# Kernel tuning notes

Hardware: AMD Instinct MI355X
Metric: run time of the kernel (lower is better)

Reference implementation:

```python
import jax, jax.numpy as jnp
import numpy as np

H = 4  # attention heads


def _lstm(x, Wih, Whh, b, reverse=False):
    # x: [N, L, din] -> hidden sequence [N, L, dh]; PyTorch gate order i,f,g,o
    if reverse:
        x = x[:, ::-1, :]
    xT = jnp.swapaxes(x, 0, 1)  # [L, N, din]
    dh = Whh.shape[1]
    N = x.shape[0]

    def step(carry, xt):
        h, c = carry
        z = xt @ Wih.T + h @ Whh.T + b
        i, f, g, o = jnp.split(z, 4, axis=-1)
        c = jax.nn.sigmoid(f) * c + jax.nn.sigmoid(i) * jnp.tanh(g)
        h = jax.nn.sigmoid(o) * jnp.tanh(c)
        return (h, c), h

    h0 = jnp.zeros((N, dh), x.dtype)
    _, hs = jax.lax.scan(step, (h0, h0), xT)
    hs = jnp.swapaxes(hs, 0, 1)
    if reverse:
        hs = hs[:, ::-1, :]
    return hs


def setup_inputs() -> dict:
    key = jax.random.key(0)
    ks = jax.random.split(key, 24)
    B, T, D = 8, 128, 512
    C, L, U, V, E = 1000, 8, 16, 5000, 256

    def w(k, shape, fan_in):
        return jax.random.normal(k, shape, jnp.float32) * (1.0 / np.sqrt(fan_in))

    inp = {
        'model_embed': jax.random.normal(ks[0], (B, T, D), jnp.float32),
        'emb_table': w(ks[1], (V, E), E),
        'ctx_Wih_f': w(ks[2], (4 * E, E), E),
        'ctx_Whh_f': w(ks[3], (4 * E, E), E),
        'ctx_b_f': jnp.zeros((4 * E,), jnp.float32),
        'ctx_Wih_b': w(ks[4], (4 * E, E), E),
        'ctx_Whh_b': w(ks[5], (4 * E, E), E),
        'ctx_b_b': jnp.zeros((4 * E,), jnp.float32),
        'ctx_out_W': w(ks[6], (D, 2 * E), 2 * E),
        'hist_Wih': w(ks[7], (4 * D, D), D),
        'hist_Whh': w(ks[8], (4 * D, D), D),
        'hist_b': jnp.zeros((4 * D,), jnp.float32),
        'hist_out_W': w(ks[9], (D, D), D),
        'Wq': w(ks[10], (D, D), D),
        'Wk': w(ks[11], (D, D), D),
        'Wv': w(ks[12], (D, D), D),
        'Wo': w(ks[13], (D, D), D),
        'acoustic_W': w(ks[14], (D, D), D),
        'context_idxs': jax.random.randint(ks[15], (C, L), 0, V),
        'context_history_idx': jax.random.randint(ks[16], (B, U), 0, C),
        'context_ilens': jax.random.randint(ks[17], (C,), 1, L + 1),
        'context_history_ilens': jax.random.randint(ks[18], (B,), 1, U + 1),
    }
    return inp


def reference(model_embed, emb_table, ctx_Wih_f, ctx_Whh_f, ctx_b_f,
              ctx_Wih_b, ctx_Whh_b, ctx_b_b, ctx_out_W,
              hist_Wih, hist_Whh, hist_b, hist_out_W,
              Wq, Wk, Wv, Wo, acoustic_W,
              context_idxs, context_history_idx, context_ilens,
              context_history_ilens):
    C, L = context_idxs.shape
    B, T, D = model_embed.shape
    U = context_history_idx.shape[1]

    # --- ContextEncoderBiLSTM: embed -> BiLSTM -> proj -> length-masked mean ---
    emb = emb_table[context_idxs]                               # [C, L, E]
    hf = _lstm(emb, ctx_Wih_f, ctx_Whh_f, ctx_b_f)
    hb = _lstm(emb, ctx_Wih_b, ctx_Whh_b, ctx_b_b, reverse=True)
    seq = jnp.concatenate([hf, hb], -1) @ ctx_out_W.T           # [C, L, D]
    m = (jnp.arange(L)[None, :] < context_ilens[:, None]).astype(seq.dtype)
    ctx_mean = (seq * m[..., None]).sum(1) / context_ilens[:, None].astype(seq.dtype)  # [C, D]

    # --- history gather + ContextHistoryEncoderLSTM ---
    hist_in = ctx_mean[context_history_idx.reshape(-1)].reshape(B, U, D)
    hist = _lstm(hist_in, hist_Wih, hist_Whh, hist_b) @ hist_out_W.T  # [B, U, D]

    # --- fuse acoustic + history, attention-based adapter ---
    mp = model_embed @ acoustic_W.T                             # [B, T, D]
    fused = (mp[:, :, None, :] + hist[:, None, :, :]).reshape(B, T * U, D)
    dh = D // H
    q = (fused @ Wq.T).reshape(B, T * U, H, dh)
    k = (ctx_mean @ Wk.T).reshape(C, H, dh)
    v = (ctx_mean @ Wv.T).reshape(C, H, dh)
    scores = jnp.einsum('bqhd,chd->bhqc', q, k) / jnp.sqrt(jnp.asarray(dh, q.dtype))
    attn = jax.nn.softmax(scores, axis=-1)                      # [B, H, TU, C]
    out = (jnp.einsum('bhqc,chd->bqhd', attn, v).reshape(B, T * U, D) @ Wo.T)
    out = out.reshape(B, T, U, D)
    prob = attn.reshape(B, H, T, U, C).mean(1)                  # [B, T, U, C]
    logit = scores.reshape(B, H, T, U, C).mean(1)

    # --- batch greedy monotonic decoding (scan over T, full length) ---
    probT = jnp.moveaxis(prob, 1, 0)                            # [T, B, U, C]
    outT = jnp.moveaxis(out, 1, 0)                              # [T, B, U, D]
    b_idx = jnp.arange(B)

    def step(u, inp):
        p_t, o_t = inp
        u_c = jnp.minimum(u, U - 1)
        valid_u = jnp.minimum(u + 1, U - 1)
        tok = context_history_idx[b_idx, valid_u]
        blank_p = p_t[b_idx, u_c, 0]
        tok_p = p_t[b_idx, u_c, tok]
        upd = (tok_p > blank_p).astype(jnp.int32)
        return u_c + upd, (u_c, o_t[b_idx, u_c])

    u0 = jnp.zeros((B,), jnp.int32)
    _, (idx, o) = jax.lax.scan(step, u0, (probT, outT))
    o = jnp.moveaxis(o, 0, 1)                                   # [B, T, D]
    return o, logit, prob
```

## Files before the change

kernel.cpp:

```cpp
#include <hip/hip_runtime.h>
#include <math.h>

namespace {
constexpr int B_ = 8, T_ = 128, D_ = 512, C_ = 1000, L_ = 8, U_ = 16, E_ = 256, H_ = 4;
constexpr int VOC_ = 5000;
constexpr int DH_ = D_ / H_;
constexpr int E4_ = 4 * E_;
constexpr int D4_ = 4 * D_;
constexpr int TU_ = T_ * U_;
constexpr int HC_ = H_ * C_;
constexpr float SCALE_ = 0.088388347648318447f;

constexpr int XZ_NB  = E4_ / 64;
constexpr int XZ_MB  = (VOC_ + 63) / 64;
constexpr int XZ_NWG = XZ_NB * XZ_MB;
constexpr int XZ_CPX = XZ_NWG / 8;

constexpr size_t XZ_    = 0;
constexpr size_t SM_    = 0;
constexpr size_t SH_    = SM_ + (size_t)B_ * T_ * HC_;
constexpr size_t AOUT_  = SH_ + (size_t)B_ * U_ * HC_;
constexpr size_t PVP_   = AOUT_ + (size_t)B_ * T_ * D_;
constexpr size_t REG_A  = 2ul * VOC_ * E4_;
constexpr size_t HPING  = REG_A;
constexpr size_t CST    = HPING + 2ul * C_ * E_;
constexpr size_t HPONG  = CST + 2ul * C_ * E_;
constexpr size_t HFALL  = HPONG + 2ul * C_ * E_;
constexpr size_t HBALL  = HFALL + (size_t)C_ * L_ * E_;
constexpr size_t CATM   = HBALL + (size_t)C_ * L_ * E_;
constexpr size_t CTXM   = CATM + (size_t)C_ * 2 * E_;
constexpr size_t KWS    = CTXM + (size_t)C_ * D_;
constexpr size_t VWS    = KWS + (size_t)C_ * D_;
constexpr size_t WQA    = VWS + (size_t)C_ * D_;
constexpr size_t WQH    = WQA + (size_t)D_ * D_;
constexpr size_t HXP    = WQH + (size_t)D_ * D_;
constexpr size_t HALL   = HXP + (size_t)B_ * U_ * D4_;
constexpr size_t HGLOB  = HALL + (size_t)B_ * U_ * D_;
constexpr size_t HG2    = HGLOB + (size_t)B_ * D_;
constexpr size_t HISTC  = HG2 + (size_t)B_ * D_;
constexpr size_t QM_    = HISTC + (size_t)B_ * D_;
constexpr size_t QH_    = QM_ + (size_t)B_ * T_ * D_;
constexpr size_t SMSUM  = QH_ + (size_t)B_ * U_ * D_;
constexpr size_t SHSUM  = SMSUM + (size_t)B_ * T_ * C_;
constexpr size_t DEN_   = SHSUM + (size_t)B_ * U_ * C_;
constexpr size_t BITS_  = DEN_ + (size_t)B_ * T_ * U_ * H_;
constexpr size_t USEL_  = BITS_ + 4096;
constexpr size_t PERM_  = USEL_ + (size_t)B_ * T_;
constexpr size_t NACT_  = PERM_ + C_;
constexpr size_t WS_NEED = NACT_ + 8;
}

__device__ __forceinline__ float fsig(float x)  { return 1.f / (1.f + __expf(-x)); }
__device__ __forceinline__ float ftanh(float x) { return 1.f - 2.f / (__expf(2.f * x) + 1.f); }
__device__ __forceinline__ void fma4(float4& a, float w, const float4& v) {
  a.x += w * v.x; a.y += w * v.y; a.z += w * v.z; a.w += w * v.w;
}

struct GemmP {
  const float* A1; int lda1;
  const int* ridx; int ridx_stride; int ridx_off;
  const float* W1; int ldw1;
  const float* bias;
  float* out; int ldc;
  int M, N, K;
  float scale;
  int a_zoff, w_zoff, c_zoff;
};

template <int TN>
__device__ __forceinline__ void gemm_core(const GemmP& g, int z, int by, int bx) {
  constexpr int UN = TN / 16;
  constexpr int WP = TN / 64;
  __shared__ float As[16][68];
  __shared__ float Ws[16][TN + 4];
  const int m0 = by * 64;
  const int n0 = bx * TN;
  if (m0 >= g.M || n0 >= g.N) return;
  const float* A1 = g.A1 + (long)z * g.a_zoff;
  const float* W1 = g.W1 + (long)z * g.w_zoff;
  float* out = g.out + (long)z * g.c_zoff;
  const int tid = threadIdx.x;
  const int tx = tid & 15, ty = tid >> 4;
  const int sr = tid >> 2, skq = (tid & 3) * 4;
  float acc[4][UN] = {};
  int sarow = -1;
  {
    const int gm = m0 + sr;
    if (gm < g.M) sarow = g.ridx ? g.ridx[gm * g.ridx_stride + g.ridx_off] : gm;
  }
  float4 pa, pw[WP];
  {
    pa = make_float4(0.f, 0.f, 0.f, 0.f);
    if (sarow >= 0) pa = *(const float4*)&A1[(long)sarow * g.lda1 + skq];
#pragma unroll
    for (int p = 0; p < WP; ++p) {
      const int gn = n0 + sr + p * 64;
      pw[p] = make_float4(0.f, 0.f, 0.f, 0.f);
      if (gn < g.N) pw[p] = *(const float4*)&W1[(long)gn * g.ldw1 + skq];
    }
  }
  for (int k0 = 0; k0 < g.K; k0 += 16) {
    As[skq][sr] = pa.x; As[skq + 1][sr] = pa.y; As[skq + 2][sr] = pa.z; As[skq + 3][sr] = pa.w;
#pragma unroll
    for (int p = 0; p < WP; ++p) {
      const int r = sr + p * 64;
      Ws[skq][r] = pw[p].x; Ws[skq + 1][r] = pw[p].y; Ws[skq + 2][r] = pw[p].z; Ws[skq + 3][r] = pw[p].w;
    }
    __syncthreads();
    const int kn = k0 + 16;
    if (kn < g.K) {
      pa = make_float4(0.f, 0.f, 0.f, 0.f);
      if (sarow >= 0) pa = *(const float4*)&A1[(long)sarow * g.lda1 + kn + skq];
#pragma unroll
      for (int p = 0; p < WP; ++p) {
        const int gn = n0 + sr + p * 64;
        pw[p] = make_float4(0.f, 0.f, 0.f, 0.f);
        if (gn < g.N) pw[p] = *(const float4*)&W1[(long)gn * g.ldw1 + kn + skq];
      }
    }
#pragma unroll
    for (int k = 0; k < 16; ++k) {
      const float4 a = *(const float4*)&As[k][ty * 4];
#pragma unroll
      for (int q = 0; q < UN / 4; ++q) {
        const float4 w = *(const float4*)&Ws[k][q * 64 + tx * 4];
        acc[0][q*4+0] += a.x * w.x; acc[0][q*4+1] += a.x * w.y; acc[0][q*4+2] += a.x * w.z; acc[0][q*4+3] += a.x * w.w;
        acc[1][q*4+0] += a.y * w.x; acc[1][q*4+1] += a.y * w.y; acc[1][q*4+2] += a.y * w.z; acc[1][q*4+3] += a.y * w.w;
        acc[2][q*4+0] += a.z * w.x; acc[2][q*4+1] += a.z * w.y; acc[2][q*4+2] += a.z * w.z; acc[2][q*4+3] += a.z * w.w;
        acc[3][q*4+0] += a.w * w.x; acc[3][q*4+1] += a.w * w.y; acc[3][q*4+2] += a.w * w.z; acc[3][q*4+3] += a.w * w.w;
      }
    }
    __syncthreads();
  }
#pragma unroll
  for (int i = 0; i < 4; ++i) {
    const int gm = m0 + ty * 4 + i;
    if (gm >= g.M) continue;
#pragma unroll
    for (int q = 0; q < UN / 4; ++q) {
#pragma unroll
      for (int j = 0; j < 4; ++j) {
        const int gn = n0 + q * 64 + tx * 4 + j;
        if (gn >= g.N) continue;
        float v2 = acc[i][q*4+j];
        if (g.bias) v2 += g.bias[gn];
        out[(long)gm * g.ldc + gn] = v2 * g.scale;
      }
    }
  }
}

__global__ __launch_bounds__(256) void k_gemm64(GemmP p)  { gemm_core<64>(p, blockIdx.z, blockIdx.y, blockIdx.x); }
__global__ __launch_bounds__(256) void k_gemm64x2(GemmP p0, GemmP p1, int zs) {
  int z = blockIdx.z;
  if (z < zs) gemm_core<64>(p0, z, blockIdx.y, blockIdx.x);
  else gemm_core<64>(p1, z - zs, blockIdx.y, blockIdx.x);
}
__global__ __launch_bounds__(256) void k_gemm64x3(GemmP p0, GemmP p1, GemmP p2) {
  int z = blockIdx.z;
  if (z == 0) gemm_core<64>(p0, 0, blockIdx.y, blockIdx.x);
  else if (z == 1) gemm_core<64>(p1, 0, blockIdx.y, blockIdx.x);
  else gemm_core<64>(p2, 0, blockIdx.y, blockIdx.x);
}
__global__ __launch_bounds__(256) void k_gemm128x2(GemmP p0, GemmP p1, int zs) {
  int z = blockIdx.z;
  if (z < zs) gemm_core<128>(p0, z, blockIdx.y, blockIdx.x);
  else gemm_core<128>(p1, z - zs, blockIdx.y, blockIdx.x);
}
__global__ __launch_bounds__(256) void k_gemm64xcd(GemmP p0, GemmP p1) {
  const int bid = blockIdx.x;
  const int logical = (bid & 7) * XZ_CPX + (bid >> 3);
  const int bx = logical % XZ_NB;
  const int by = logical / XZ_NB;
  if (blockIdx.z == 0) gemm_core<64>(p0, 0, by, bx);
  else gemm_core<64>(p1, 0, by, bx);
}

__global__ __launch_bounds__(256) void k_gemm_nn(
    const float* __restrict__ A0, const float* __restrict__ B0, float* __restrict__ O0,
    const float* __restrict__ A1, const float* __restrict__ B1, float* __restrict__ O1) {
  const float* A = blockIdx.z ? A1 : A0;
  const float* B = blockIdx.z ? B1 : B0;
  float* O = blockIdx.z ? O1 : O0;
  __shared__ float As[16][68];
  __shared__ float Bs[16][68];
  const int m0 = blockIdx.y * 64, n0 = blockIdx.x * 64;
  const int tid = threadIdx.x;
  const int tx = tid & 15, ty = tid >> 4;
  const int sr = tid >> 2, skq = (tid & 3) * 4;
  float acc[4][4] = {};
  for (int k0 = 0; k0 < 512; k0 += 16) {
    {
      float4 v = *(const float4*)&A[(long)(m0 + sr) * 512 + k0 + skq];
      As[skq][sr] = v.x; As[skq + 1][sr] = v.y; As[skq + 2][sr] = v.z; As[skq + 3][sr] = v.w;
    }
#pragma unroll
    for (int p = 0; p < 4; ++p) {
      int idx = tid + p * 256;
      int kk = idx >> 6, jj = idx & 63;
      Bs[kk][jj] = B[(long)(k0 + kk) * 512 + n0 + jj];
    }
    __syncthreads();
#pragma unroll
    for (int k = 0; k < 16; ++k) {
      const float4 a = *(const float4*)&As[k][ty * 4];
      const float4 w = *(const float4*)&Bs[k][tx * 4];
      acc[0][0] += a.x * w.x; acc[0][1] += a.x * w.y; acc[0][2] += a.x * w.z; acc[0][3] += a.x * w.w;
      acc[1][0] += a.y * w.x; acc[1][1] += a.y * w.y; acc[1][2] += a.y * w.z; acc[1][3] += a.y * w.w;
      acc[2][0] += a.z * w.x; acc[2][1] += a.z * w.y; acc[2][2] += a.z * w.z; acc[2][3] += a.z * w.w;
      acc[3][0] += a.w * w.x; acc[3][1] += a.w * w.y; acc[3][2] += a.w * w.z; acc[3][3] += a.w * w.w;
    }
    __syncthreads();
  }
#pragma unroll
  for (int i = 0; i < 4; ++i)
#pragma unroll
    for (int j = 0; j < 4; ++j)
      O[(long)(m0 + ty * 4 + i) * 512 + n0 + tx * 4 + j] = acc[i][j];
}

__global__ __launch_bounds__(256) void k_perm(
    const int* __restrict__ ilens, int* __restrict__ perm, int* __restrict__ nact) {
  __shared__ int cnt[9];
  __shared__ int start[9];
  const int tid = threadIdx.x;
  if (tid < 9) cnt[tid] = 0;
  __syncthreads();
  for (int c = tid; c < C_; c += 256) atomicAdd(&cnt[ilens[c]], 1);
  __syncthreads();
  if (tid == 0) {
    int acc = 0;
    for (int k = 8; k >= 0; --k) { start[k] = acc; if (k > 0) acc += cnt[k]; }
    for (int t = 0; t < 8; ++t) nact[t] = start[t];
  }
  __syncthreads();
  const int wave = tid >> 6, lane = tid & 63;
  for (int k = wave + 1; k <= 8; k += 4) {
    int base = start[k];
    for (int c0 = 0; c0 < C_; c0 += 64) {
      int c = c0 + lane;
      bool f = (c < C_) && (ilens[c] == k);
      unsigned long long m = __ballot(f);
      if (f) {
        int r = __popcll(m & ((1ull << lane) - 1ull));
        perm[base + r] = c;
      }
      base += __popcll(m);
    }
  }
}

__global__ __launch_bounds__(256) void k_ctx_step(
    const float* __restrict__ xz, const int* __restrict__ ctx_idxs,
    const float* __restrict__ Whh_f, const float* __restrict__ Whh_b,
    const float* __restrict__ h_prev, float* __restrict__ h_next,
    float* __restrict__ c_st,
    float* __restrict__ hf_all, float* __restrict__ hb_all,
    const int* __restrict__ perm, const int* __restrict__ nactArr, int t) {
  __shared__ float Hs[32][20];
  __shared__ float Wg[4][32][68];
  __shared__ float zb[4][16][68];
  const int e0 = blockIdx.x * 64;
  const int c0 = blockIdx.y * 16;
  const int dir = blockIdx.z;
  int nact = C_;
  if (dir == 0) {
    nact = nactArr[t];
    if (c0 >= nact) return;
  }
  const int tid = threadIdx.x;
  const float* Whh = dir ? Whh_b : Whh_f;
  const float* hp = h_prev + (size_t)dir * C_ * E_;
  const int gp = tid >> 7;
  const int rem = tid & 127;
  const int cy = rem >> 4;
  const int ex = rem & 15;
  const bool hstage = (tid < 128);
  const int hcr = tid & 15, hkq = ((tid >> 4) & 7) * 4;
  const int hc = c0 + hcr;
  int hrow = -1;
  if (dir == 0) { if (hc < nact) hrow = perm[hc]; }
  else if (hc < C_) hrow = hc;
  float4 acc4[2][2];
  acc4[0][0] = acc4[0][1] = acc4[1][0] = acc4[1][1] = make_float4(0.f, 0.f, 0.f, 0.f);
  float4 phv = make_float4(0.f, 0.f, 0.f, 0.f);
  float4 pwv[8];
  if (hstage && hrow >= 0) phv = *(const float4*)&hp[(size_t)hrow * E_ + hkq];
#pragma unroll
  for (int p = 0; p < 8; ++p) {
    int idx = tid + p * 256;
    int ee = idx & 63, kq = ((idx >> 6) & 7) * 4, gg = idx >> 9;
    pwv[p] = *(const float4*)&Whh[(size_t)(gg * E_ + e0 + ee) * E_ + kq];
  }
  for (int k0 = 0; k0 < E_; k0 += 32) {
    if (hstage) {
      Hs[hkq][hcr] = phv.x; Hs[hkq + 1][hcr] = phv.y; Hs[hkq + 2][hcr] = phv.z; Hs[hkq + 3][hcr] = phv.w;
    }
#pragma unroll
    for (int p = 0; p < 8; ++p) {
      int idx = tid + p * 256;
      int ee = idx & 63, kq = ((idx >> 6) & 7) * 4, gg = idx >> 9;
      Wg[gg][kq][ee] = pwv[p].x; Wg[gg][kq + 1][ee] = pwv[p].y; Wg[gg][kq + 2][ee] = pwv[p].z; Wg[gg][kq + 3][ee] = pwv[p].w;
    }
    __syncthreads();
    const int kn = k0 + 32;
    if (kn < E_) {
      phv = make_float4(0.f, 0.f, 0.f, 0.f);
      if (hstage && hrow >= 0) phv = *(const float4*)&hp[(size_t)hrow * E_ + kn + hkq];
#pragma unroll
      for (int p = 0; p < 8; ++p) {
        int idx = tid + p * 256;
        int ee = idx & 63, kq = ((idx >> 6) & 7) * 4, gg = idx >> 9;
        pwv[p] = *(const float4*)&Whh[(size_t)(gg * E_ + e0 + ee) * E_ + kn + kq];
      }
    }
#pragma unroll
    for (int kk = 0; kk < 32; ++kk) {
      const float a0 = Hs[kk][cy * 2];
      const float a1 = Hs[kk][cy * 2 + 1];
#pragma unroll
      for (int gg = 0; gg < 2; ++gg) {
        const float4 w = *(const float4*)&Wg[gp * 2 + gg][kk][ex * 4];
        fma4(acc4[gg][0], a0, w);
        fma4(acc4[gg][1], a1, w);
      }
    }
    __syncthreads();
  }
#pragma unroll
  for (int gg = 0; gg < 2; ++gg) {
    *(float4*)&zb[gp * 2 + gg][cy * 2 + 0][ex * 4] = acc4[gg][0];
    *(float4*)&zb[gp * 2 + gg][cy * 2 + 1][ex * 4] = acc4[gg][1];
  }
  __syncthreads();
  const int lpos = dir ? (L_ - 1 - t) : t;
  const float* xz_dir = xz + (size_t)dir * VOC_ * E4_;
  float* c_state = c_st + (size_t)dir * C_ * E_;
  float* hn_out = h_next + (size_t)dir * C_ * E_;
  float* hall = dir ? hb_all : hf_all;
  const int oc = tid >> 4, oe = (tid & 15) * 4;
  const int lc = c0 + oc;
  int c = -1;
  if (dir == 0) { if (lc < nact) c = perm[lc]; }
  else if (lc < C_) c = lc;
  if (c >= 0) {
    const int e = e0 + oe;
    const int tok = ctx_idxs[c * L_ + lpos];
    const float* xr = xz_dir + (size_t)tok * E4_;
    float zi[4], zf[4], zg[4], zo[4], cp[4], cn[4], hn[4];
    *(float4*)zi = *(const float4*)&xr[e];
    *(float4*)zf = *(const float4*)&xr[E_ + e];
    *(float4*)zg = *(const float4*)&xr[2 * E_ + e];
    *(float4*)zo = *(const float4*)&xr[3 * E_ + e];
    *(float4*)cp = *(const float4*)&c_state[(size_t)c * E_ + e];
#pragma unroll
    for (int j = 0; j < 4; ++j) {
      float vi = zi[j] + zb[0][oc][oe + j];
      float vf = zf[j] + zb[1][oc][oe + j];
      float vg = zg[j] + zb[2][oc][oe + j];
      float vo = zo[j] + zb[3][oc][oe + j];
      cn[j] = fsig(vf) * cp[j] + fsig(vi) * ftanh(vg);
      hn[j] = fsig(vo) * ftanh(cn[j]);
    }
    *(float4*)&c_state[(size_t)c * E_ + e] = *(float4*)cn;
    *(float4*)&hn_out[(size_t)c * E_ + e] = *(float4*)hn;
    *(float4*)&hall[((size_t)c * L_ + lpos) * E_ + e] = *(float4*)hn;
  }
}

__global__ __launch_bounds__(256) void k_ctx_mean(
    const float* __restrict__ hf_all, const float* __restrict__ hb_all,
    const int* __restrict__ ilens, float* __restrict__ cat_mean) {
  int idx = blockIdx.x * 256 + threadIdx.x;
  if (idx >= C_ * 2 * E_) return;
  int c = idx / (2 * E_), e = idx - c * 2 * E_;
  const float* src = (e < E_) ? hf_all : hb_all;
  int ee = e & (E_ - 1);
  int il = ilens[c];
  float s = 0.f;
#pragma unroll
  for (int l = 0; l < L_; ++l)
    if (l < il) s += src[((size_t)c * L_ + l) * E_ + ee];
  cat_mean[idx] = s / (float)il;
}

__global__ __launch_bounds__(256) void k_hist_step2(
    const float* __restrict__ xproj, const float* __restrict__ Whh,
    const float* __restrict__ hprev, float* __restrict__ hcur,
    float* __restrict__ cstG, float* __restrict__ hall, int u) {
  __shared__ float Wl[32][516];
  __shared__ float hb[8][520];
  const int tid = threadIdx.x;
  const int e0 = blockIdx.x * 8;
  {
    int lr = tid >> 3, part = tid & 7;
    int g2 = lr >> 3, e2 = lr & 7;
    const float* src = Whh + (size_t)(g2 * D_ + e0 + e2) * D_;
#pragma unroll
    for (int i = 0; i < 16; ++i) {
      int k4 = part + i * 8;
      *(float4*)&Wl[lr][k4 * 4] = *(const float4*)&src[k4 * 4];
    }
  }
  {
    int b2 = tid >> 5, part = tid & 31;
#pragma unroll
    for (int i = 0; i < 4; ++i) {
      int k4 = part + i * 32;
      float4 v = make_float4(0.f, 0.f, 0.f, 0.f);
      if (u > 0) v = *(const float4*)&hprev[(size_t)b2 * D_ + k4 * 4];
      *(float4*)&hb[b2][k4 * 4] = v;
    }
  }
  __syncthreads();
  const int b = tid >> 5, g = (tid >> 3) & 3, e = tid & 7;
  const int lr = tid & 31;
  float dot = 0.f;
#pragma unroll 8
  for (int k4 = 0; k4 < 128; ++k4) {
    float4 w = *(const float4*)&Wl[lr][k4 * 4];
    float4 h4 = *(const float4*)&hb[b][k4 * 4];
    dot += w.x * h4.x + w.y * h4.y + w.z * h4.z + w.w * h4.w;
  }
  float z = dot + xproj[((size_t)b * U_ + u) * D4_ + g * D_ + e0 + e];
  const int l = tid & 63;
  const int base = (l & 32) | e;
  float zi = __shfl(z, base, 64);
  float zf = __shfl(z, base + 8, 64);
  float zg = __shfl(z, base + 16, 64);
  float zo = __shfl(z, base + 24, 64);
  if (g == 0) {
    float cp = (u > 0) ? cstG[(size_t)b * D_ + e0 + e] : 0.f;
    float cn = fsig(zf) * cp + fsig(zi) * ftanh(zg);
    cstG[(size_t)b * D_ + e0 + e] = cn;
    float hv = fsig(zo) * ftanh(cn);
    hcur[(size_t)b * D_ + e0 + e] = hv;
    hall[((size_t)b * U_ + u) * D_ + e0 + e] = hv;
  }
}

__global__ __launch_bounds__(256) void k_rowexp(
    float* __restrict__ Sm, float* __restrict__ Sh,
    float* __restrict__ SmS, float* __restrict__ ShS) {
  int row = blockIdx.x;
  float* base; float* sumo;
  if (row < B_ * T_) { base = Sm + (size_t)row * HC_; sumo = SmS + (size_t)row * C_; }
  else { int r2 = row - B_ * T_; base = Sh + (size_t)r2 * HC_; sumo = ShS + (size_t)r2 * C_; }
  int tid = threadIdx.x;
  for (int c = tid; c < C_; c += 256) {
    float s = base[c] + base[C_ + c] + base[2 * C_ + c] + base[3 * C_ + c];
    sumo[c] = 0.25f * s;
  }
  __syncthreads();
  int h = tid >> 6, lane = tid & 63;
  float* p = base + (size_t)h * C_;
  float mx = -1e30f;
  for (int c = lane; c < C_; c += 64) mx = fmaxf(mx, p[c]);
#pragma unroll
  for (int o = 32; o; o >>= 1) mx = fmaxf(mx, __shfl_xor(mx, o));
  for (int c = lane; c < C_; c += 64) p[c] = __expf(p[c] - mx);
}

__global__ __launch_bounds__(256) void k_plw(
    const float* __restrict__ EM, const float* __restrict__ EH,
    const float* __restrict__ SmS, const float* __restrict__ ShS,
    const int* __restrict__ hidx,
    float* __restrict__ den, float* __restrict__ prob, float* __restrict__ logit,
    unsigned char* __restrict__ bits) {
  __shared__ float sEM[H_][1008];
  __shared__ float sSS[1000];
  __shared__ float sB[4], sT[4];
  __shared__ float sW[4][4];
  __shared__ float sInvU[4];
  const int bt = blockIdx.x >> 2;
  const int ug = blockIdx.x & 3;
  const int b = bt >> 7;
  const int tid = threadIdx.x;
  for (int i = tid; i < H_ * C_; i += 256) sEM[i / C_][i % C_] = EM[(size_t)bt * HC_ + i];
  for (int c = tid; c < C_; c += 256) sSS[c] = SmS[(size_t)bt * C_ + c];
  __syncthreads();
#pragma unroll
  for (int j = 0; j < 4; ++j) {
    const int u = ug * 4 + j;
    const int valid = (u + 1 < U_ - 1) ? (u + 1) : (U_ - 1);
    const int tok = hidx[b * U_ + valid];
    const float* eh0 = EH + ((size_t)b * U_ + u) * HC_;
    float d0 = 0.f, d1 = 0.f, d2 = 0.f, d3 = 0.f;
    for (int c = tid; c < C_; c += 256) {
      d0 += sEM[0][c] * eh0[c];
      d1 += sEM[1][c] * eh0[C_ + c];
      d2 += sEM[2][c] * eh0[2 * C_ + c];
      d3 += sEM[3][c] * eh0[3 * C_ + c];
    }
#pragma unroll
    for (int o = 32; o; o >>= 1) {
      d0 += __shfl_xor(d0, o); d1 += __shfl_xor(d1, o);
      d2 += __shfl_xor(d2, o); d3 += __shfl_xor(d3, o);
    }
    const int wv = tid >> 6;
    if ((tid & 63) == 0) { sW[wv][0] = d0; sW[wv][1] = d1; sW[wv][2] = d2; sW[wv][3] = d3; }
    __syncthreads();
    if (tid < 4) {
      float dd = sW[0][tid] + sW[1][tid] + sW[2][tid] + sW[3][tid];
      den[((size_t)bt * U_ + u) * H_ + tid] = dd;
      sInvU[tid] = 0.25f / dd;
    }
    __syncthreads();
    const float i0 = sInvU[0], i1 = sInvU[1], i2 = sInvU[2], i3 = sInvU[3];
    const float* shs = ShS + ((size_t)b * U_ + u) * C_;
    size_t obase = ((size_t)bt * U_ + u) * C_;
    for (int c = tid; c < C_; c += 256) {
      float pr = sEM[0][c] * eh0[c] * i0 + sEM[1][c] * eh0[C_ + c] * i1
               + sEM[2][c] * eh0[2 * C_ + c] * i2 + sEM[3][c] * eh0[3 * C_ + c] * i3;
      __builtin_nontemporal_store(pr, &prob[obase + c]);
      __builtin_nontemporal_store(sSS[c] + shs[c], &logit[obase + c]);
      if (c == 0) sB[j] = pr;
      if (c == tok) sT[j] = pr;
    }
    __syncthreads();
  }
  if (tid < 4) bits[bt * U_ + ug * 4 + tid] = (sT[tid] > sB[tid]) ? 1 : 0;
}

__global__ __launch_bounds__(64) void k_scan(
    const unsigned char* __restrict__ bits, int* __restrict__ u_sel) {
  __shared__ unsigned char sb[B_ * T_ * U_];
  int tid = threadIdx.x;
  for (int i = tid; i < B_ * T_ * U_; i += 64) sb[i] = bits[i];
  __syncthreads();
  if (tid < B_) {
    int u = 0;
    for (int t = 0; t < T_; ++t) {
      int uc = (u < U_ - 1) ? u : (U_ - 1);
      u_sel[tid * T_ + t] = uc;
      u = uc + (int)sb[(tid * T_ + t) * U_ + uc];
    }
  }
}

__global__ __launch_bounds__(256) void k_pvg2(
    const float* __restrict__ EM, const float* __restrict__ EH,
    const float* __restrict__ den, const int* __restrict__ u_sel,
    const float* __restrict__ vmat, float* __restrict__ pvp) {
  constexpr int KC = 64;
  __shared__ float wS[2][4][4][KC + 4];
  __shared__ float invS[8][4];
  __shared__ int bS[8], tS[8], uS[8];
  const int tid = threadIdx.x;
  const int cblk = blockIdx.y;
  if (tid < 32) {
    int g8 = tid >> 2, hh = tid & 3;
    int bt = blockIdx.x * 8 + g8;
    int b = bt >> 7, t = bt & 127;
    int u = u_sel[bt];
    if (hh == 0) { bS[g8] = b; tS[g8] = t; uS[g8] = u; }
    invS[g8][hh] = 1.f / den[((size_t)bt * U_ + u) * H_ + hh];
  }
  __syncthreads();
  const int sub = tid >> 7, lt = tid & 127;
  const int d = lt * 4;
  const int h = lt >> 5;
  float4 acc[4];
  acc[0] = acc[1] = acc[2] = acc[3] = make_float4(0.f, 0.f, 0.f, 0.f);
  const int cbeg = cblk * 128;
  const int cend = (cbeg + 128 < C_) ? (cbeg + 128) : C_;
  for (int c0 = cbeg; c0 < cend; c0 += KC) {
#pragma unroll
    for (int p = 0; p < 8; ++p) {
      int idx = tid + p * 256;
      int cc = idx & 63;
      int rest = idx >> 6;
      int hh = rest & 3, gg = (rest >> 2) & 3, ss = rest >> 4;
      int g8 = ss * 4 + gg;
      int c = c0 + cc;
      float w = 0.f;
      if (c < C_) {
        int b = bS[g8], t = tS[g8], u = uS[g8];
        float em = EM[(((size_t)b * T_ + t) * H_ + hh) * C_ + c];
        float eh = EH[(((size_t)b * U_ + u) * H_ + hh) * C_ + c];
        w = em * eh * invS[g8][hh];
      }
      wS[ss][gg][hh][cc] = w;
    }
    __syncthreads();
#pragma unroll 4
    for (int q = 0; q < KC / 4; ++q) {
      const float4 w0 = *(const float4*)&wS[sub][0][h][q * 4];
      const float4 w1 = *(const float4*)&wS[sub][1][h][q * 4];
      const float4 w2 = *(const float4*)&wS[sub][2][h][q * 4];
      const float4 w3 = *(const float4*)&wS[sub][3][h][q * 4];
      int c = c0 + q * 4;
      float4 v;
      if (c < C_) { v = *(const float4*)&vmat[(size_t)c * D_ + d];
        fma4(acc[0], w0.x, v); fma4(acc[1], w1.x, v); fma4(acc[2], w2.x, v); fma4(acc[3], w3.x, v); }
      if (c + 1 < C_) { v = *(const float4*)&vmat[(size_t)(c + 1) * D_ + d];
        fma4(acc[0], w0.y, v); fma4(acc[1], w1.y, v); fma4(acc[2], w2.y, v); fma4(acc[3], w3.y, v); }
      if (c + 2 < C_) { v = *(const float4*)&vmat[(size_t)(c + 2) * D_ + d];
        fma4(acc[0], w0.z, v); fma4(acc[1], w1.z, v); fma4(acc[2], w2.z, v); fma4(acc[3], w3.z, v); }
      if (c + 3 < C_) { v = *(const float4*)&vmat[(size_t)(c + 3) * D_ + d];
        fma4(acc[0], w0.w, v); fma4(acc[1], w1.w, v); fma4(acc[2], w2.w, v); fma4(acc[3], w3.w, v); }
    }
    __syncthreads();
  }
  float* pout = pvp + (size_t)cblk * (B_ * T_) * D_;
#pragma unroll
  for (int g = 0; g < 4; ++g) {
    int bt = (bS[sub * 4 + g] << 7) + tS[sub * 4 + g];
    *(float4*)&pout[(size_t)bt * D_ + d] = acc[g];
  }
}

__global__ __launch_bounds__(256) void k_pvred(
    const float* __restrict__ pvp, float* __restrict__ aout) {
  const size_t i = ((size_t)blockIdx.x * 256 + threadIdx.x) * 4;
  float4 s = *(const float4*)&pvp[i];
#pragma unroll
  for (int k = 1; k < 8; ++k) {
    const float4 v = *(const float4*)&pvp[(size_t)k * (B_ * T_) * D_ + i];
    s.x += v.x; s.y += v.y; s.z += v.z; s.w += v.w;
  }
  *(float4*)&aout[i] = s;
}

extern "C" void kernel_launch(void* const* d_in, const int* in_sizes, int n_in,
                              void* d_out, int out_size, void* d_ws, size_t ws_size,
                              hipStream_t stream) {
  const float* model_embed = (const float*)d_in[0];
  const float* emb_table   = (const float*)d_in[1];
  const float* Wih_f = (const float*)d_in[2];
  const float* Whh_f = (const float*)d_in[3];
  const float* b_f   = (const float*)d_in[4];
  const float* Wih_b = (const float*)d_in[5];
  const float* Whh_b = (const float*)d_in[6];
  const float* b_b   = (const float*)d_in[7];
  const float* ctx_out_W  = (const float*)d_in[8];
  const float* hist_Wih   = (const float*)d_in[9];
  const float* hist_Whh   = (const float*)d_in[10];
  const float* hist_b     = (const float*)d_in[11];
  const float* hist_out_W = (const float*)d_in[12];
  const float* Wq = (const float*)d_in[13];
  const float* Wk = (const float*)d_in[14];
  const float* Wv = (const float*)d_in[15];
  const float* Wo = (const float*)d_in[16];
  const float* acoustic_W = (const float*)d_in[17];
  const int* ctx_idxs = (const int*)d_in[18];
  const int* hidx     = (const int*)d_in[19];
  const int* ilens    = (const int*)d_in[20];

  if (ws_size < WS_NEED * sizeof(float)) return;

  float* ws = (float*)d_ws;
  float* o_out     = (float*)d_out;
  float* logit_out = o_out + (size_t)B_ * T_ * D_;
  float* prob_out  = logit_out + (size_t)B_ * T_ * U_ * C_;

  hipMemsetAsync(ws + HPING, 0, 4ul * C_ * E_ * sizeof(float), stream);

  k_perm<<<dim3(1), 256, 0, stream>>>(ilens, (int*)(ws + PERM_), (int*)(ws + NACT_));

  k_gemm_nn<<<dim3(8, 8, 2), 256, 0, stream>>>(
      Wq, acoustic_W, ws + WQA, Wq, hist_out_W, ws + WQH);

  {
    GemmP pf{};
    pf.A1 = emb_table; pf.lda1 = E_;
    pf.W1 = Wih_f; pf.ldw1 = E_;
    pf.bias = b_f;
    pf.out = ws + XZ_; pf.ldc = E4_;
    pf.M = VOC_; pf.N = E4_; pf.K = E_; pf.scale = 1.f;
    GemmP pb = pf;
    pb.W1 = Wih_b; pb.bias = b_b; pb.out = ws + XZ_ + (size_t)VOC_ * E4_;
    k_gemm64xcd<<<dim3(XZ_NWG, 1, 2), 256, 0, stream>>>(pf, pb);
  }

  for (int t = 0; t < L_; ++t) {
    float* hp = ws + ((t & 1) ? HPONG : HPING);
    float* hn = ws + ((t & 1) ? HPING : HPONG);
    k_ctx_step<<<dim3(4, (C_ + 15) / 16, 2), 256, 0, stream>>>(
        ws + XZ_, ctx_idxs, Whh_f, Whh_b, hp, hn, ws + CST,
        ws + HFALL, ws + HBALL,
        (const int*)(ws + PERM_), (const int*)(ws + NACT_), t);
  }

  k_ctx_mean<<<dim3((C_ * 2 * E_ + 255) / 256), 256, 0, stream>>>(
      ws + HFALL, ws + HBALL, ilens, ws + CATM);
  {
    GemmP p{};
    p.A1 = ws + CATM; p.lda1 = 2 * E_;
    p.W1 = ctx_out_W; p.ldw1 = 2 * E_;
    p.out = ws + CTXM; p.ldc = D_; p.M = C_; p.N = D_; p.K = 2 * E_; p.scale = 1.f;
    k_gemm64<<<dim3(8, 16, 1), 256, 0, stream>>>(p);
  }

  {
    GemmP pk{};
    pk.A1 = ws + CTXM; pk.lda1 = D_;
    pk.W1 = Wk; pk.ldw1 = D_;
    pk.out = ws + KWS; pk.ldc = D_; pk.M = C_; pk.N = D_; pk.K = D_; pk.scale = SCALE_;
    GemmP pv = pk;
    pv.W1 = Wv; pv.out = ws + VWS; pv.scale = 1.f;
    GemmP ph{};
    ph.A1 = ws + CTXM; ph.lda1 = D_;
    ph.ridx = hidx; ph.ridx_stride = 1; ph.ridx_off = 0;
    ph.W1 = hist_Wih; ph.ldw1 = D_;
    ph.bias = hist_b;
    ph.out = ws + HXP; ph.ldc = D4_; ph.M = B_ * U_; ph.N = D4_; ph.K = D_; ph.scale = 1.f;
    k_gemm64x3<<<dim3(32, 16, 3), 256, 0, stream>>>(pk, pv, ph);
  }

  for (int u = 0; u < U_; ++u) {
    const float* hp = ws + ((u & 1) ? HG2 : HGLOB);
    float* hc = ws + ((u & 1) ? HGLOB : HG2);
    k_hist_step2<<<dim3(64), 256, 0, stream>>>(
        ws + HXP, hist_Whh, hp, hc, ws + HISTC, ws + HALL, u);
  }

  {
    GemmP pm{};
    pm.A1 = model_embed; pm.lda1 = D_;
    pm.W1 = ws + WQA; pm.ldw1 = D_;
    pm.out = ws + QM_; pm.ldc = D_; pm.M = B_ * T_; pm.N = D_; pm.K = D_; pm.scale = 1.f;
    GemmP ph = pm;
    ph.A1 = ws + HALL; ph.W1 = ws + WQH; ph.out = ws + QH_; ph.M = B_ * U_;
    k_gemm64x2<<<dim3(8, 16, 2), 256, 0, stream>>>(pm, ph, 1);
  }

  {
    GemmP pm{};
    pm.A1 = ws + QM_; pm.lda1 = D_;
    pm.W1 = ws + KWS; pm.ldw1 = D_;
    pm.out = ws + SM_; pm.ldc = HC_; pm.M = B_ * T_; pm.N = C_; pm.K = DH_; pm.scale = 1.f;
    pm.a_zoff = DH_; pm.w_zoff = DH_; pm.c_zoff = C_;
    GemmP ph = pm;
    ph.A1 = ws + QH_; ph.out = ws + SH_; ph.M = B_ * U_;
    k_gemm128x2<<<dim3(8, 16, 8), 256, 0, stream>>>(pm, ph, 4);
  }

  k_rowexp<<<dim3(B_ * T_ + B_ * U_), 256, 0, stream>>>(
      ws + SM_, ws + SH_, ws + SMSUM, ws + SHSUM);

  k_plw<<<dim3(B_ * T_ * 4), 256, 0, stream>>>(
      ws + SM_, ws + SH_, ws + SMSUM, ws + SHSUM, hidx,
      ws + DEN_, prob_out, logit_out, (unsigned char*)(ws + BITS_));

  k_scan<<<dim3(1), 64, 0, stream>>>((const unsigned char*)(ws + BITS_), (int*)(ws + USEL_));

  k_pvg2<<<dim3(128, 8), 256, 0, stream>>>(
      ws + SM_, ws + SH_, ws + DEN_, (const int*)(ws + USEL_), ws + VWS, ws + PVP_);
  k_pvred<<<dim3((B_ * T_ * D_) / (256 * 4)), 256, 0, stream>>>(ws + PVP_, ws + AOUT_);

  {
    GemmP p{};
    p.A1 = ws + AOUT_; p.lda1 = D_;
    p.W1 = Wo; p.ldw1 = D_;
    p.out = o_out; p.ldc = D_; p.M = B_ * T_; p.N = D_; p.K = D_; p.scale = 1.f;
    k_gemm64<<<dim3(8, 16, 1), 256, 0, stream>>>(p);
  }
}
```

Before: 760.1 us.

## Fuse partial-sum reduction into Wo GEMM, batch Q-proj GEMM, drop memset

Replaces the separate k_pvred reduction and Wo GEMM with one kernel that sums the 8 partial slabs while loading A tiles. The model-embed query projection moves into the earlier batched K/V/hist-input GEMM launch, and only the small history-query GEMM stays after the history LSTM. The ctx LSTM step now skips loading h and c at t=0 and uses zeros instead, so the workspace memset can go. Together these cut several launches and intermediate traffic. The cost is 8x redundant slab reads per N-tile in the fused GEMM.

After: 797.9 us. 1.05x slower.

```diff
diff --git a/kernel.cpp b/kernel.cpp
--- a/kernel.cpp
+++ b/kernel.cpp
@@ -48,6 +48,7 @@
 constexpr size_t PERM_  = USEL_ + (size_t)B_ * T_;
 constexpr size_t NACT_  = PERM_ + C_;
 constexpr size_t WS_NEED = NACT_ + 8;
+constexpr size_t PVSLAB = (size_t)B_ * T_ * D_;
 }
 
 __device__ __forceinline__ float fsig(float x)  { return 1.f / (1.f + __expf(-x)); }
@@ -151,16 +152,12 @@
 }
 
 __global__ __launch_bounds__(256) void k_gemm64(GemmP p)  { gemm_core<64>(p, blockIdx.z, blockIdx.y, blockIdx.x); }
-__global__ __launch_bounds__(256) void k_gemm64x2(GemmP p0, GemmP p1, int zs) {
-  int z = blockIdx.z;
-  if (z < zs) gemm_core<64>(p0, z, blockIdx.y, blockIdx.x);
-  else gemm_core<64>(p1, z - zs, blockIdx.y, blockIdx.x);
-}
-__global__ __launch_bounds__(256) void k_gemm64x3(GemmP p0, GemmP p1, GemmP p2) {
+__global__ __launch_bounds__(256) void k_gemm64x4(GemmP p0, GemmP p1, GemmP p2, GemmP p3) {
   int z = blockIdx.z;
   if (z == 0) gemm_core<64>(p0, 0, blockIdx.y, blockIdx.x);
   else if (z == 1) gemm_core<64>(p1, 0, blockIdx.y, blockIdx.x);
-  else gemm_core<64>(p2, 0, blockIdx.y, blockIdx.x);
+  else if (z == 2) gemm_core<64>(p2, 0, blockIdx.y, blockIdx.x);
+  else gemm_core<64>(p3, 0, blockIdx.y, blockIdx.x);
 }
 __global__ __launch_bounds__(256) void k_gemm128x2(GemmP p0, GemmP p1, int zs) {
   int z = blockIdx.z;
@@ -174,6 +171,51 @@
   const int by = logical / XZ_NB;
   if (blockIdx.z == 0) gemm_core<64>(p0, 0, by, bx);
   else gemm_core<64>(p1, 0, by, bx);
+}
+
+__global__ __launch_bounds__(256) void k_wo_red8(
+    const float* __restrict__ pvp, const float* __restrict__ W,
+    float* __restrict__ out) {
+  __shared__ float As[16][68];
+  __shared__ float Ws[16][68];
+  const int m0 = blockIdx.y * 64, n0 = blockIdx.x * 64;
+  const int tid = threadIdx.x;
+  const int tx = tid & 15, ty = tid >> 4;
+  const int sr = tid >> 2, skq = (tid & 3) * 4;
+  float acc[4][4] = {};
+  const float* arow = pvp + (long)(m0 + sr) * D_;
+  const float* wrow = W + (long)(n0 + sr) * D_;
+  for (int k0 = 0; k0 < D_; k0 += 16) {
+    {
+      float4 s = *(const float4*)&arow[k0 + skq];
+#pragma unroll
+      for (int k = 1; k < 8; ++k) {
+        const float4 v = *(const float4*)&arow[(size_t)k * PVSLAB + k0 + skq];
+        s.x += v.x; s.y += v.y; s.z += v.z; s.w += v.w;
+      }
+      As[skq][sr] = s.x; As[skq + 1][sr] = s.y; As[skq + 2][sr] = s.z; As[skq + 3][sr] = s.w;
+    }
+    {
+      float4 w = *(const float4*)&wrow[k0 + skq];
+      Ws[skq][sr] = w.x; Ws[skq + 1][sr] = w.y; Ws[skq + 2][sr] = w.z; Ws[skq + 3][sr] = w.w;
+    }
+    __syncthreads();
+#pragma unroll
+    for (int k = 0; k < 16; ++k) {
+      const float4 a = *(const float4*)&As[k][ty * 4];
+      const float4 w = *(const float4*)&Ws[k][tx * 4];
+      acc[0][0] += a.x * w.x; acc[0][1] += a.x * w.y; acc[0][2] += a.x * w.z; acc[0][3] += a.x * w.w;
+      acc[1][0] += a.y * w.x; acc[1][1] += a.y * w.y; acc[1][2] += a.y * w.z; acc[1][3] += a.y * w.w;
+      acc[2][0] += a.z * w.x; acc[2][1] += a.z * w.y; acc[2][2] += a.z * w.z; acc[2][3] += a.z * w.w;
+      acc[3][0] += a.w * w.x; acc[3][1] += a.w * w.y; acc[3][2] += a.w * w.z; acc[3][3] += a.w * w.w;
+    }
+    __syncthreads();
+  }
+#pragma unroll
+  for (int i = 0; i < 4; ++i)
+#pragma unroll
+    for (int j = 0; j < 4; ++j)
+      out[(long)(m0 + ty * 4 + i) * D_ + n0 + tx * 4 + j] = acc[i][j];
 }
 
 __global__ __launch_bounds__(256) void k_gemm_nn(
@@ -281,11 +323,12 @@
   int hrow = -1;
   if (dir == 0) { if (hc < nact) hrow = perm[hc]; }
   else if (hc < C_) hrow = hc;
+  const bool loadH = (t > 0);
   float4 acc4[2][2];
   acc4[0][0] = acc4[0][1] = acc4[1][0] = acc4[1][1] = make_float4(0.f, 0.f, 0.f, 0.f);
   float4 phv = make_float4(0.f, 0.f, 0.f, 0.f);
   float4 pwv[8];
-  if (hstage && hrow >= 0) phv = *(const float4*)&hp[(size_t)hrow * E_ + hkq];
+  if (hstage && hrow >= 0 && loadH) phv = *(const float4*)&hp[(size_t)hrow * E_ + hkq];
 #pragma unroll
   for (int p = 0; p < 8; ++p) {
     int idx = tid + p * 256;
@@ -306,7 +349,7 @@
     const int kn = k0 + 32;
     if (kn < E_) {
       phv = make_float4(0.f, 0.f, 0.f, 0.f);
-      if (hstage && hrow >= 0) phv = *(const float4*)&hp[(size_t)hrow * E_ + kn + hkq];
+      if (hstage && hrow >= 0 && loadH) phv = *(const float4*)&hp[(size_t)hrow * E_ + kn + hkq];
 #pragma unroll
       for (int p = 0; p < 8; ++p) {
         int idx = tid + p * 256;
@@ -352,7 +395,8 @@
     *(float4*)zf = *(const float4*)&xr[E_ + e];
     *(float4*)zg = *(const float4*)&xr[2 * E_ + e];
     *(float4*)zo = *(const float4*)&xr[3 * E_ + e];
-    *(float4*)cp = *(const float4*)&c_state[(size_t)c * E_ + e];
+    if (loadH) *(float4*)cp = *(const float4*)&c_state[(size_t)c * E_ + e];
+    else { cp[0] = cp[1] = cp[2] = cp[3] = 0.f; }
 #pragma unroll
     for (int j = 0; j < 4; ++j) {
       float vi = zi[j] + zb[0][oc][oe + j];
@@ -602,24 +646,12 @@
     }
     __syncthreads();
   }
-  float* pout = pvp + (size_t)cblk * (B_ * T_) * D_;
+  float* pout = pvp + (size_t)cblk * PVSLAB;
 #pragma unroll
   for (int g = 0; g < 4; ++g) {
     int bt = (bS[sub * 4 + g] << 7) + tS[sub * 4 + g];
     *(float4*)&pout[(size_t)bt * D_ + d] = acc[g];
   }
-}
-
-__global__ __launch_bounds__(256) void k_pvred(
-    const float* __restrict__ pvp, float* __restrict__ aout) {
-  const size_t i = ((size_t)blockIdx.x * 256 + threadIdx.x) * 4;
-  float4 s = *(const float4*)&pvp[i];
-#pragma unroll
-  for (int k = 1; k < 8; ++k) {
-    const float4 v = *(const float4*)&pvp[(size_t)k * (B_ * T_) * D_ + i];
-    s.x += v.x; s.y += v.y; s.z += v.z; s.w += v.w;
-  }
-  *(float4*)&aout[i] = s;
 }
 
 extern "C" void kernel_launch(void* const* d_in, const int* in_sizes, int n_in,
@@ -654,8 +686,6 @@
   float* logit_out = o_out + (size_t)B_ * T_ * D_;
   float* prob_out  = logit_out + (size_t)B_ * T_ * U_ * C_;
 
-  hipMemsetAsync(ws + HPING, 0, 4ul * C_ * E_ * sizeof(float), stream);
-
   k_perm<<<dim3(1), 256, 0, stream>>>(ilens, (int*)(ws + PERM_), (int*)(ws + NACT_));
 
   k_gemm_nn<<<dim3(8, 8, 2), 256, 0, stream>>>(
@@ -705,7 +735,11 @@
     ph.W1 = hist_Wih; ph.ldw1 = D_;
     ph.bias = hist_b;
     ph.out = ws + HXP; ph.ldc = D4_; ph.M = B_ * U_; ph.N = D4_; ph.K = D_; ph.scale = 1.f;
-    k_gemm64x3<<<dim3(32, 16, 3), 256, 0, stream>>>(pk, pv, ph);
+    GemmP pm{};
+    pm.A1 = model_embed; pm.lda1 = D_;
+    pm.W1 = ws + WQA; pm.ldw1 = D_;
+    pm.out = ws + QM_; pm.ldc = D_; pm.M = B_ * T_; pm.N = D_; pm.K = D_; pm.scale = 1.f;
+    k_gemm64x4<<<dim3(32, 16, 4), 256, 0, stream>>>(pk, pv, ph, pm);
   }
 
   for (int u = 0; u < U_; ++u) {
@@ -716,13 +750,11 @@
   }
 
   {
-    GemmP pm{};
-    pm.A1 = model_embed; pm.lda1 = D_;
-    pm.W1 = ws + WQA; pm.ldw1 = D_;
-    pm.out = ws + QM_; pm.ldc = D_; pm.M = B_ * T_; pm.N = D_; pm.K = D_; pm.scale = 1.f;
-    GemmP ph = pm;
-    ph.A1 = ws + HALL; ph.W1 = ws + WQH; ph.out = ws + QH_; ph.M = B_ * U_;
-    k_gemm64x2<<<dim3(8, 16, 2), 256, 0, stream>>>(pm, ph, 1);
+    GemmP ph{};
+    ph.A1 = ws + HALL; ph.lda1 = D_;
+    ph.W1 = ws + WQH; ph.ldw1 = D_;
+    ph.out = ws + QH_; ph.ldc = D_; ph.M = B_ * U_; ph.N = D_; ph.K = D_; ph.scale = 1.f;
+    k_gemm64<<<dim3(8, 2, 1), 256, 0, stream>>>(ph);
   }
 
   {
@@ -747,13 +779,6 @@
 
   k_pvg2<<<dim3(128, 8), 256, 0, stream>>>(
       ws + SM_, ws + SH_, ws + DEN_, (const int*)(ws + USEL_), ws + VWS, ws + PVP_);
-  k_pvred<<<dim3((B_ * T_ * D_) / (256 * 4)), 256, 0, stream>>>(ws + PVP_, ws + AOUT_);
-
-  {
-    GemmP p{};
-    p.A1 = ws + AOUT_; p.lda1 = D_;
-    p.W1 = Wo; p.ldw1 = D_;
-    p.out = o_out; p.ldc = D_; p.M = B_ * T_; p.N = D_; p.K = D_; p.scale = 1.f;
-    k_gemm64<<<dim3(8, 16, 1), 256, 0, stream>>>(p);
-  }
-}
+
+  k_wo_red8<<<dim3(8, 16), 256, 0, stream>>>(ws + PVP_, Wo, o_out);
+}
```
